# Optimization experiments

Hardware: AMD Instinct MI355X
Metric: run time of the kernel (lower is better)

## Reference

```python
import jax, jax.numpy as jnp
import numpy as np

HIDDEN = 15
DEPTH = 6  # total hidden conv layers: 1 (k=2) + (DEPTH-1) (k=1)
CLIP = 1.0


def setup_inputs() -> dict:
    key = jax.random.key(0)
    ks = jax.random.split(key, 8)
    B, X = 1024, 8192
    rho_BX = jax.random.uniform(ks[0], (B, X), dtype=jnp.float32)
    # first conv: kernel_size=2, in=1, out=HIDDEN -> weight (HIDDEN, 2)
    # kaiming_normal for relu: std = sqrt(2 / fan_in), fan_in = in_ch*k = 2
    w0 = jax.random.normal(ks[1], (HIDDEN, 2), dtype=jnp.float32) * np.sqrt(2.0 / 2.0)
    b0 = jnp.zeros((HIDDEN,), dtype=jnp.float32)
    # hidden 1x1 convs: (DEPTH-1) layers of (HIDDEN, HIDDEN)
    Wh = jax.random.normal(ks[2], (DEPTH - 1, HIDDEN, HIDDEN), dtype=jnp.float32) * np.sqrt(2.0 / HIDDEN)
    bh = jnp.zeros((DEPTH - 1, HIDDEN), dtype=jnp.float32)
    # final 1x1 conv: out=1 -> weight (HIDDEN,)
    Wl = jax.random.normal(ks[3], (HIDDEN,), dtype=jnp.float32) * np.sqrt(2.0 / HIDDEN)
    bl = jnp.zeros((1,), dtype=jnp.float32)
    return {"rho_BX": rho_BX, "w0": w0, "b0": b0, "Wh": Wh, "bh": bh, "Wl": Wl, "bl": bl}


def reference(rho_BX, w0, b0, Wh, bh, Wl, bl):
    # first conv (kernel=2, no padding): pairs of adjacent densities
    # h[b, x, c] = w0[c,0]*rho[b,x] + w0[c,1]*rho[b,x+1] + b0[c]
    h = rho_BX[:, :-1, None] * w0[:, 0] + rho_BX[:, 1:, None] * w0[:, 1] + b0  # (B, X-1, H)
    h = jax.nn.relu(h)
    for i in range(Wh.shape[0]):  # fixed small depth: pointwise 1x1 conv layers
        h = jax.nn.relu(jnp.einsum('bxh,oh->bxo', h, Wh[i]) + bh[i])
    out = jnp.einsum('bxh,h->bx', h, Wl) + bl[0]  # (B, X-1)
    return jnp.clip(out, 0.0, CLIP)
```

## Files before the change

### kernel.cpp

```cpp
#include <hip/hip_runtime.h>

typedef __attribute__((ext_vector_type(8))) _Float16 half8;
typedef __attribute__((ext_vector_type(2))) __fp16 fp16x2;
typedef __attribute__((ext_vector_type(4))) float f32x4;

#define XDIM 8192
#define XOUT 8191
#define TPW 16
#define NTILES (1024 * 512)
#define NBLOCKS (NTILES / TPW / 4)

union H8 {
    fp16x2 p[4];
    half8 v;
};

#define MFMA32(A, B, C) __builtin_amdgcn_mfma_f32_16x16x32_f16((A), (B), (C), 0, 0, 0)

__global__ __launch_bounds__(64) void cnn_prep_kernel(
    const float* __restrict__ w0, const float* __restrict__ b0,
    const float* __restrict__ Wh, const float* __restrict__ bh,
    const float* __restrict__ Wl, void* __restrict__ ws) {
    const int lane = threadIdx.x & 63;
    const int lm = lane & 15;
    const int kb = (lane >> 4) * 4;
    const bool biaslane = (kb == 12);

    half8* wsA = (half8*)ws;
    float4* wsF = (float4*)((char*)ws + 10240);

    for (int L = 0; L < 5; ++L) {
        float _w0 = (lm < 15) ? Wh[L*225 + lm*15 + kb + 0] : 0.f;
        float _w1 = (lm < 15) ? Wh[L*225 + lm*15 + kb + 1] : 0.f;
        float _w2 = (lm < 15) ? Wh[L*225 + lm*15 + kb + 2] : 0.f;
        float _w3 = (lm < 15) ? (biaslane ? bh[L*15 + lm]
                                          : Wh[L*225 + lm*15 + kb + 3]) : 0.f;
        fp16x2 h01 = __builtin_amdgcn_cvt_pkrtz(_w0, _w1);
        fp16x2 h23 = __builtin_amdgcn_cvt_pkrtz(_w2, _w3);
        const float e0 = fmaf(-1.0f, (float)h01.x, _w0);
        const float e1 = fmaf(-1.0f, (float)h01.y, _w1);
        const float e2 = fmaf(-1.0f, (float)h23.x, _w2);
        const float e3 = fmaf(-1.0f, (float)h23.y, _w3);
        fp16x2 l01 = __builtin_amdgcn_cvt_pkrtz(e0, e1);
        fp16x2 l23 = __builtin_amdgcn_cvt_pkrtz(e2, e3);
        H8 u1, u2;
        u1.p[0] = h01; u1.p[1] = h23; u1.p[2] = h01; u1.p[3] = h23;
        fp16x2 z = __builtin_amdgcn_cvt_pkrtz(0.f, 0.f);
        u2.p[0] = l01; u2.p[1] = l23; u2.p[2] = z;   u2.p[3] = z;
        wsA[L*64 + lane] = u1.v;
        wsA[(5+L)*64 + lane] = u2.v;
    }

    float4 f0, f1, f2, f3;
    f0.x = (kb+0 < 15) ? w0[2*(kb+0)]   : 0.f;
    f0.y = (kb+1 < 15) ? w0[2*(kb+1)]   : 0.f;
    f0.z = (kb+2 < 15) ? w0[2*(kb+2)]   : 0.f;
    f0.w = (kb+3 < 15) ? w0[2*(kb+3)]   : 0.f;
    f1.x = (kb+0 < 15) ? w0[2*(kb+0)+1] : 0.f;
    f1.y = (kb+1 < 15) ? w0[2*(kb+1)+1] : 0.f;
    f1.z = (kb+2 < 15) ? w0[2*(kb+2)+1] : 0.f;
    f1.w = (kb+3 < 15) ? w0[2*(kb+3)+1] : 0.f;
    f2.x = (kb+0 < 15) ? b0[kb+0] : 0.f;
    f2.y = (kb+1 < 15) ? b0[kb+1] : 0.f;
    f2.z = (kb+2 < 15) ? b0[kb+2] : 0.f;
    f2.w = (kb+3 < 15) ? b0[kb+3] : 0.f;
    f3.x = (kb+0 < 15) ? Wl[kb+0] : 0.f;
    f3.y = (kb+1 < 15) ? Wl[kb+1] : 0.f;
    f3.z = (kb+2 < 15) ? Wl[kb+2] : 0.f;
    f3.w = (kb+3 < 15) ? Wl[kb+3] : 0.f;
    wsF[lane*4 + 0] = f0;
    wsF[lane*4 + 1] = f1;
    wsF[lane*4 + 2] = f2;
    wsF[lane*4 + 3] = f3;
}

__global__ __attribute__((amdgpu_flat_work_group_size(256, 256)))
void cnn_mfma_kernel(
    const float* __restrict__ rho, const float* __restrict__ bl,
    const void* __restrict__ ws, float* __restrict__ out) {
    const int lane = threadIdx.x & 63;
    const int lm = lane & 15;
    const int kb = (lane >> 4) * 4;
    const bool biaslane = (kb == 12);

    const half8* wsA = (const half8*)ws;
    const float4* wsF = (const float4*)((const char*)ws + 10240);

    const half8 A1_0 = wsA[0*64 + lane];
    const half8 A1_1 = wsA[1*64 + lane];
    const half8 A1_2 = wsA[2*64 + lane];
    const half8 A1_3 = wsA[3*64 + lane];
    const half8 A1_4 = wsA[4*64 + lane];
    const half8 A2_0 = wsA[5*64 + lane];
    const half8 A2_1 = wsA[6*64 + lane];
    const half8 A2_2 = wsA[7*64 + lane];
    const half8 A2_3 = wsA[8*64 + lane];
    const half8 A2_4 = wsA[9*64 + lane];
    const float4 F0 = wsF[lane*4 + 0];
    const float4 F1 = wsF[lane*4 + 1];
    const float4 F2 = wsF[lane*4 + 2];
    const float4 F3 = wsF[lane*4 + 3];
    const float bl0 = bl[0];

    const int wid = blockIdx.x * 4 + (threadIdx.x >> 6);
    const int brow = wid >> 5;
    const int xb = ((wid & 31) << 8) + lm;
    const float* rrow = rho + (size_t)brow * XDIM;
    float* orow = out + (size_t)brow * XOUT;

#pragma unroll 2
    for (int t = 0; t < TPW; ++t) {
        const int x = xb + t * 16;
        const float r0 = rrow[x];
        const float r1 = rrow[(x < XDIM - 1) ? x + 1 : XDIM - 1];

        float h0 = fmaxf(fmaf(F0.x, r0, fmaf(F1.x, r1, F2.x)), 0.f);
        float h1 = fmaxf(fmaf(F0.y, r0, fmaf(F1.y, r1, F2.y)), 0.f);
        float h2 = fmaxf(fmaf(F0.z, r0, fmaf(F1.z, r1, F2.z)), 0.f);
        float h3 = biaslane ? 1.0f
                            : fmaxf(fmaf(F0.w, r0, fmaf(F1.w, r1, F2.w)), 0.f);

#define HLAYER(A1F, A2F)                                             \
        {                                                            \
            H8 _b;                                                   \
            _b.p[0] = __builtin_amdgcn_cvt_pkrtz(h0, h1);            \
            _b.p[1] = __builtin_amdgcn_cvt_pkrtz(h2, h3);            \
            const float _e0 = fmaf(-1.0f, (float)_b.p[0].x, h0);     \
            const float _e1 = fmaf(-1.0f, (float)_b.p[0].y, h1);     \
            const float _e2 = fmaf(-1.0f, (float)_b.p[1].x, h2);     \
            const float _e3 = fmaf(-1.0f, (float)_b.p[1].y, h3);     \
            _b.p[2] = __builtin_amdgcn_cvt_pkrtz(_e0, _e1);          \
            _b.p[3] = __builtin_amdgcn_cvt_pkrtz(_e2, _e3);          \
            f32x4 _zc = {0.f, 0.f, 0.f, 0.f};                        \
            f32x4 _acc = MFMA32((A1F), _b.v, _zc);                   \
            _acc = MFMA32((A2F), _b.v, _acc);                        \
            h0 = fmaxf(_acc.x, 0.f);                                 \
            h1 = fmaxf(_acc.y, 0.f);                                 \
            h2 = fmaxf(_acc.z, 0.f);                                 \
            h3 = biaslane ? 1.0f : fmaxf(_acc.w, 0.f);               \
        }
        HLAYER(A1_0, A2_0)
        HLAYER(A1_1, A2_1)
        HLAYER(A1_2, A2_2)
        HLAYER(A1_3, A2_3)
        HLAYER(A1_4, A2_4)
#undef HLAYER

        float s = fmaf(F3.x, h0, fmaf(F3.y, h1, fmaf(F3.z, h2, F3.w * h3)));
        s += __shfl_xor(s, 16, 64);
        s += __shfl_xor(s, 32, 64);
        const float y = fminf(fmaxf(s + bl0, 0.f), 1.f);
        if (lane < 16 && x < XOUT) orow[x] = y;
    }
}

extern "C" void kernel_launch(void* const* d_in, const int* in_sizes, int n_in,
                              void* d_out, int out_size, void* d_ws, size_t ws_size,
                              hipStream_t stream) {
    const float* rho = (const float*)d_in[0];
    const float* w0  = (const float*)d_in[1];
    const float* b0  = (const float*)d_in[2];
    const float* Wh  = (const float*)d_in[3];
    const float* bh  = (const float*)d_in[4];
    const float* Wl  = (const float*)d_in[5];
    const float* bl  = (const float*)d_in[6];
    float* out = (float*)d_out;

    cnn_prep_kernel<<<1, 64, 0, stream>>>(w0, b0, Wh, bh, Wl, d_ws);
    cnn_mfma_kernel<<<NBLOCKS, 256, 0, stream>>>(rho, bl, d_ws, out);
}
```

Measured before the change: 138.2 us.

## Stage weights in LDS and fold hidden biases into MFMA accumulator init

Weights are now copied into shared memory once per block and re-read from LDS inside the loop rather than held in registers for the whole kernel, which should lower VGPR pressure and allow more waves per SIMD. The hidden-layer bias, previously carried through a constant-1 input lane, now comes in as a separate accumulator vector that seeds the MFMA. This drops the biaslane selects. The cost is extra LDS reads every iteration, a block-wide copy plus barrier at kernel start, and about 19 KB of LDS per block, which could itself limit occupancy.

After: 146.1 us. 1.06x slower.

```diff
diff --git a/kernel.cpp b/kernel.cpp
--- a/kernel.cpp
+++ b/kernel.cpp
@@ -9,6 +9,8 @@
 #define TPW 16
 #define NTILES (1024 * 512)
 #define NBLOCKS (NTILES / TPW / 4)
+
+#define WS_BYTES 19456
 
 union H8 {
     fp16x2 p[4];
@@ -24,17 +26,16 @@
     const int lane = threadIdx.x & 63;
     const int lm = lane & 15;
     const int kb = (lane >> 4) * 4;
-    const bool biaslane = (kb == 12);
 
     half8* wsA = (half8*)ws;
-    float4* wsF = (float4*)((char*)ws + 10240);
+    f32x4* wsB = (f32x4*)((char*)ws + 10240);
+    float4* wsF = (float4*)((char*)ws + 15360);
 
     for (int L = 0; L < 5; ++L) {
-        float _w0 = (lm < 15) ? Wh[L*225 + lm*15 + kb + 0] : 0.f;
-        float _w1 = (lm < 15) ? Wh[L*225 + lm*15 + kb + 1] : 0.f;
-        float _w2 = (lm < 15) ? Wh[L*225 + lm*15 + kb + 2] : 0.f;
-        float _w3 = (lm < 15) ? (biaslane ? bh[L*15 + lm]
-                                          : Wh[L*225 + lm*15 + kb + 3]) : 0.f;
+        float _w0 = (lm < 15 && kb + 0 < 15) ? Wh[L*225 + lm*15 + kb + 0] : 0.f;
+        float _w1 = (lm < 15 && kb + 1 < 15) ? Wh[L*225 + lm*15 + kb + 1] : 0.f;
+        float _w2 = (lm < 15 && kb + 2 < 15) ? Wh[L*225 + lm*15 + kb + 2] : 0.f;
+        float _w3 = (lm < 15 && kb + 3 < 15) ? Wh[L*225 + lm*15 + kb + 3] : 0.f;
         fp16x2 h01 = __builtin_amdgcn_cvt_pkrtz(_w0, _w1);
         fp16x2 h23 = __builtin_amdgcn_cvt_pkrtz(_w2, _w3);
         const float e0 = fmaf(-1.0f, (float)h01.x, _w0);
@@ -49,6 +50,13 @@
         u2.p[0] = l01; u2.p[1] = l23; u2.p[2] = z;   u2.p[3] = z;
         wsA[L*64 + lane] = u1.v;
         wsA[(5+L)*64 + lane] = u2.v;
+
+        f32x4 bv;
+        bv.x = (kb + 0 < 15) ? bh[L*15 + kb + 0] : 0.f;
+        bv.y = (kb + 1 < 15) ? bh[L*15 + kb + 1] : 0.f;
+        bv.z = (kb + 2 < 15) ? bh[L*15 + kb + 2] : 0.f;
+        bv.w = (kb + 3 < 15) ? bh[L*15 + kb + 3] : 0.f;
+        wsB[L*64 + lane] = bv;
     }
 
     float4 f0, f1, f2, f3;
@@ -68,41 +76,32 @@
     f3.y = (kb+1 < 15) ? Wl[kb+1] : 0.f;
     f3.z = (kb+2 < 15) ? Wl[kb+2] : 0.f;
     f3.w = (kb+3 < 15) ? Wl[kb+3] : 0.f;
-    wsF[lane*4 + 0] = f0;
-    wsF[lane*4 + 1] = f1;
-    wsF[lane*4 + 2] = f2;
-    wsF[lane*4 + 3] = f3;
+    wsF[0*64 + lane] = f0;
+    wsF[1*64 + lane] = f1;
+    wsF[2*64 + lane] = f2;
+    wsF[3*64 + lane] = f3;
 }
 
 __global__ __attribute__((amdgpu_flat_work_group_size(256, 256)))
 void cnn_mfma_kernel(
     const float* __restrict__ rho, const float* __restrict__ bl,
     const void* __restrict__ ws, float* __restrict__ out) {
-    const int lane = threadIdx.x & 63;
+    __shared__ char lds[WS_BYTES];
+    const int tid = threadIdx.x;
+    {
+        const float4* src = (const float4*)ws;
+        float4* dst = (float4*)lds;
+        for (int i = tid; i < WS_BYTES / 16; i += 256) dst[i] = src[i];
+    }
+    __syncthreads();
+
+    const int lane = tid & 63;
     const int lm = lane & 15;
-    const int kb = (lane >> 4) * 4;
-    const bool biaslane = (kb == 12);
+    const char* lbase = lds + lane * 16;
 
-    const half8* wsA = (const half8*)ws;
-    const float4* wsF = (const float4*)((const char*)ws + 10240);
-
-    const half8 A1_0 = wsA[0*64 + lane];
-    const half8 A1_1 = wsA[1*64 + lane];
-    const half8 A1_2 = wsA[2*64 + lane];
-    const half8 A1_3 = wsA[3*64 + lane];
-    const half8 A1_4 = wsA[4*64 + lane];
-    const half8 A2_0 = wsA[5*64 + lane];
-    const half8 A2_1 = wsA[6*64 + lane];
-    const half8 A2_2 = wsA[7*64 + lane];
-    const half8 A2_3 = wsA[8*64 + lane];
-    const half8 A2_4 = wsA[9*64 + lane];
-    const float4 F0 = wsF[lane*4 + 0];
-    const float4 F1 = wsF[lane*4 + 1];
-    const float4 F2 = wsF[lane*4 + 2];
-    const float4 F3 = wsF[lane*4 + 3];
     const float bl0 = bl[0];
 
-    const int wid = blockIdx.x * 4 + (threadIdx.x >> 6);
+    const int wid = blockIdx.x * 4 + (tid >> 6);
     const int brow = wid >> 5;
     const int xb = ((wid & 31) << 8) + lm;
     const float* rrow = rho + (size_t)brow * XDIM;
@@ -114,38 +113,44 @@
         const float r0 = rrow[x];
         const float r1 = rrow[(x < XDIM - 1) ? x + 1 : XDIM - 1];
 
+        const float4 F0 = *(const float4*)(lbase + 15360 + 0*1024);
+        const float4 F1 = *(const float4*)(lbase + 15360 + 1*1024);
+        const float4 F2 = *(const float4*)(lbase + 15360 + 2*1024);
+
         float h0 = fmaxf(fmaf(F0.x, r0, fmaf(F1.x, r1, F2.x)), 0.f);
         float h1 = fmaxf(fmaf(F0.y, r0, fmaf(F1.y, r1, F2.y)), 0.f);
         float h2 = fmaxf(fmaf(F0.z, r0, fmaf(F1.z, r1, F2.z)), 0.f);
-        float h3 = biaslane ? 1.0f
-                            : fmaxf(fmaf(F0.w, r0, fmaf(F1.w, r1, F2.w)), 0.f);
+        float h3 = fmaxf(fmaf(F0.w, r0, fmaf(F1.w, r1, F2.w)), 0.f);
 
-#define HLAYER(A1F, A2F)                                             \
-        {                                                            \
-            H8 _b;                                                   \
-            _b.p[0] = __builtin_amdgcn_cvt_pkrtz(h0, h1);            \
-            _b.p[1] = __builtin_amdgcn_cvt_pkrtz(h2, h3);            \
-            const float _e0 = fmaf(-1.0f, (float)_b.p[0].x, h0);     \
-            const float _e1 = fmaf(-1.0f, (float)_b.p[0].y, h1);     \
-            const float _e2 = fmaf(-1.0f, (float)_b.p[1].x, h2);     \
-            const float _e3 = fmaf(-1.0f, (float)_b.p[1].y, h3);     \
-            _b.p[2] = __builtin_amdgcn_cvt_pkrtz(_e0, _e1);          \
-            _b.p[3] = __builtin_amdgcn_cvt_pkrtz(_e2, _e3);          \
-            f32x4 _zc = {0.f, 0.f, 0.f, 0.f};                        \
-            f32x4 _acc = MFMA32((A1F), _b.v, _zc);                   \
-            _acc = MFMA32((A2F), _b.v, _acc);                        \
-            h0 = fmaxf(_acc.x, 0.f);                                 \
-            h1 = fmaxf(_acc.y, 0.f);                                 \
-            h2 = fmaxf(_acc.z, 0.f);                                 \
-            h3 = biaslane ? 1.0f : fmaxf(_acc.w, 0.f);               \
+#define HLAYER(L)                                                     \
+        {                                                             \
+            const half8 _A1 = *(const half8*)(lbase + (L)*1024);      \
+            const half8 _A2 = *(const half8*)(lbase + (5+(L))*1024);  \
+            const f32x4 _BV = *(const f32x4*)(lbase + 10240 + (L)*1024); \
+            H8 _b;                                                    \
+            _b.p[0] = __builtin_amdgcn_cvt_pkrtz(h0, h1);             \
+            _b.p[1] = __builtin_amdgcn_cvt_pkrtz(h2, h3);             \
+            const float _e0 = fmaf(-1.0f, (float)_b.p[0].x, h0);      \
+            const float _e1 = fmaf(-1.0f, (float)_b.p[0].y, h1);      \
+            const float _e2 = fmaf(-1.0f, (float)_b.p[1].x, h2);      \
+            const float _e3 = fmaf(-1.0f, (float)_b.p[1].y, h3);      \
+            _b.p[2] = __builtin_amdgcn_cvt_pkrtz(_e0, _e1);           \
+            _b.p[3] = __builtin_amdgcn_cvt_pkrtz(_e2, _e3);           \
+            f32x4 _acc = MFMA32(_A1, _b.v, _BV);                      \
+            _acc = MFMA32(_A2, _b.v, _acc);                           \
+            h0 = fmaxf(_acc.x, 0.f);                                  \
+            h1 = fmaxf(_acc.y, 0.f);                                  \
+            h2 = fmaxf(_acc.z, 0.f);                                  \
+            h3 = fmaxf(_acc.w, 0.f);                                  \
         }
-        HLAYER(A1_0, A2_0)
-        HLAYER(A1_1, A2_1)
-        HLAYER(A1_2, A2_2)
-        HLAYER(A1_3, A2_3)
-        HLAYER(A1_4, A2_4)
+        HLAYER(0)
+        HLAYER(1)
+        HLAYER(2)
+        HLAYER(3)
+        HLAYER(4)
 #undef HLAYER
 
+        const float4 F3 = *(const float4*)(lbase + 15360 + 3*1024);
         float s = fmaf(F3.x, h0, fmaf(F3.y, h1, fmaf(F3.z, h2, F3.w * h3)));
         s += __shfl_xor(s, 16, 64);
         s += __shfl_xor(s, 32, 64);
```
